# Kernel optimization log

Hardware: AMD Instinct MI355X
Metric: run time of the kernel (lower is better)

## Reference

```python
import jax, jax.numpy as jnp
import numpy as np

N, E = 10000, 80000
D, D_EDGE, L = 32, 16, 3
D2 = D * D


def layer_norm(x, g, b, eps=1e-5):
    m = jnp.mean(x, axis=-1, keepdims=True)
    v = jnp.var(x, axis=-1, keepdims=True)
    return (x - m) / jnp.sqrt(v + eps) * g + b


def setup_inputs() -> dict:
    key = jax.random.key(0)
    ks = jax.random.split(key, 16)
    s_e = 1.0 / np.sqrt(D_EDGE)
    s_d = 1.0 / np.sqrt(D)
    s_f = 1.0 / np.sqrt(L * D)
    return {
        "x": jax.random.normal(ks[0], (N, D), dtype=jnp.float32),
        "edge_index": jax.random.randint(ks[1], (2, E), 0, N),
        "edge_attr": jax.random.normal(ks[2], (E, D_EDGE), dtype=jnp.float32),
        # shared edge MLP: Linear(d_edge_in -> d^2) + LayerNorm(d^2) + ReLU
        "emlp_w": jax.random.uniform(ks[3], (D2, D_EDGE), jnp.float32, -s_e, s_e),
        "emlp_b": jnp.zeros((D2,), jnp.float32),
        "emlp_ln_g": jnp.ones((D2,), jnp.float32),
        "emlp_ln_b": jnp.zeros((D2,), jnp.float32),
        # per-layer params (stacked over L layers)
        "root_w": jax.random.uniform(ks[4], (L, D, D), jnp.float32, -s_d, s_d),  # NNConv root lin (no bias)
        "conv_b": jnp.zeros((L, D), jnp.float32),                                # NNConv bias
        "res_w": jax.random.uniform(ks[5], (L, D, D), jnp.float32, -s_d, s_d),
        "res_b": jnp.zeros((L, D), jnp.float32),
        "ln_g": jnp.ones((L, D), jnp.float32),
        "ln_b": jnp.zeros((L, D), jnp.float32),
        # fusion: Linear(L*d -> d) + LayerNorm(d) + ReLU
        "fuse_w": jax.random.uniform(ks[6], (D, L * D), jnp.float32, -s_f, s_f),
        "fuse_b": jnp.zeros((D,), jnp.float32),
        "fuse_ln_g": jnp.ones((D,), jnp.float32),
        "fuse_ln_b": jnp.zeros((D,), jnp.float32),
    }


def reference(x, edge_index, edge_attr, emlp_w, emlp_b, emlp_ln_g, emlp_ln_b,
              root_w, conv_b, res_w, res_b, ln_g, ln_b,
              fuse_w, fuse_b, fuse_ln_g, fuse_ln_b):
    n_nodes = x.shape[0]
    src, tgt = edge_index[0], edge_index[1]
    # Shared edge MLP applied to the same edge_attr in every layer -> identical
    # per-edge weight matrices; compute once. [E, d_in, d_out]
    h = layer_norm(edge_attr @ emlp_w.T + emlp_b, emlp_ln_g, emlp_ln_b)
    We = jax.nn.relu(h).reshape(-1, D, D)
    x_src_gatherer = src
    outputs = []
    for l in range(L):
        x_res = x @ res_w[l].T + res_b[l]
        # NNConv message: x_j @ W_e, scatter-add to target nodes
        msg = jnp.einsum('ed,edf->ef', x[x_src_gatherer], We)  # [E, d]
        agg = jax.ops.segment_sum(msg, tgt, num_segments=n_nodes)
        h = agg + x @ root_w[l].T + conv_b[l]
        # dropout is identity in eval mode
        x = layer_norm(h + x_res, ln_g[l], ln_b[l])
        outputs.append(x)
    fused = jnp.concatenate(outputs, axis=-1) @ fuse_w.T + fuse_b
    fused = jax.nn.relu(layer_norm(fused, fuse_ln_g, fuse_ln_b))
    return fused
```

## Files before the change

kernel.cpp:

```cpp
#include <hip/hip_runtime.h>

#define NN 10000
#define EE 80000
#define DD 32
#define DEDGE 16
#define LL 3
#define D2V 1024
#define NTILE 2500

typedef __attribute__((ext_vector_type(8))) short short8v;
typedef __attribute__((ext_vector_type(16))) float f32x16;

__device__ __forceinline__ unsigned short bf16rne(float x) {
    unsigned u = __float_as_uint(x);
    return (unsigned short)((u + 0x7FFF + ((u >> 16) & 1)) >> 16);
}
__device__ __forceinline__ float bf16tof(unsigned short h) {
    return __uint_as_float(((unsigned)h) << 16);
}
__device__ __forceinline__ uint4 pack8(const unsigned short* u) {
    uint4 r;
    r.x = (unsigned)u[0] | ((unsigned)u[1] << 16);
    r.y = (unsigned)u[2] | ((unsigned)u[3] << 16);
    r.z = (unsigned)u[4] | ((unsigned)u[5] << 16);
    r.w = (unsigned)u[6] | ((unsigned)u[7] << 16);
    return r;
}

__global__ __launch_bounds__(1024) void setup_kernel(
    const int* __restrict__ ei,
    const float* __restrict__ emw, const float* __restrict__ emb,
    const float* __restrict__ elg, const float* __restrict__ elb,
    int* __restrict__ cur, int* __restrict__ off, float* __restrict__ st,
    uint4* __restrict__ afh, uint4* __restrict__ afl, uint4* __restrict__ a2f)
{
    __shared__ int smi[NN + 1024];
    const int bid = blockIdx.x;
    const int t = threadIdx.x;

    if (bid == 0) {
        int* cnt = smi;
        int* part = smi + NN;
        for (int i = t; i < NN; i += 1024) cnt[i] = 0;
        __syncthreads();
        for (int e = t; e < EE; e += 1024) atomicAdd(&cnt[ei[EE + e]], 1);
        __syncthreads();
        const int base = t * 10;
        int loc[10];
        int run = 0;
#pragma unroll
        for (int i = 0; i < 10; ++i) {
            const int idx = base + i;
            const int v = (idx < NN) ? cnt[idx] : 0;
            loc[i] = run;
            run += v;
        }
        part[t] = run;
        __syncthreads();
        for (int o = 1; o < 1024; o <<= 1) {
            const int v = (t >= o) ? part[t - o] : 0;
            __syncthreads();
            part[t] += v;
            __syncthreads();
        }
        const int excl = part[t] - run;
#pragma unroll
        for (int i = 0; i < 10; ++i) {
            const int idx = base + i;
            if (idx < NN) {
                off[idx] = excl + loc[i];
                cur[idx] = excl + loc[i];
            }
        }
        if (t == 1023) off[NN] = part[1023];
    } else if (bid == 1) {
        float* ws = (float*)smi;
        float* bs = ((float*)smi) + 2048;
        float accM = 0.f, s = 0.f, q = 0.f, sb = 0.f, sb2 = 0.f;
        for (int c = 0; c < 8; ++c) {
            const int r0 = c * 128;
            for (int i = t; i < 2048; i += 1024) ws[i] = emw[r0 * DEDGE + i];
            if (t < 128) bs[t] = emb[r0 + t];
            __syncthreads();
            if (t < 256) {
                const int k = t >> 4, j = t & 15;
                for (int r = 0; r < 128; ++r)
                    accM = fmaf(ws[r * 16 + k], ws[r * 16 + j], accM);
            } else if (t < 272) {
                const int kk = t - 256;
                for (int r = 0; r < 128; ++r) {
                    s += ws[r * 16 + kk];
                    q = fmaf(bs[r], ws[r * 16 + kk], q);
                }
            } else if (t == 288) {
                for (int r = 0; r < 128; ++r) {
                    sb += bs[r];
                    sb2 = fmaf(bs[r], bs[r], sb2);
                }
            }
            __syncthreads();
        }
        if (t < 256) {
            st[t] = accM * (1.f / D2V);
        } else if (t < 272) {
            st[t] = s * (1.f / D2V);
            st[t + 16] = q * (1.f / D2V);
        } else if (t == 288) {
            st[288] = sb * (1.f / D2V);
            st[289] = sb2 * (1.f / D2V);
        }
    } else {
        const int tid2 = (bid - 2) * 1024 + t;
        const int d = tid2 >> 6, l = tid2 & 63;
        const int row = l & 31, kh = l >> 5;
        const int r = d * 32 + row;
        const float g = elg[r];
        unsigned short uh[8], ul[8];
#pragma unroll
        for (int i = 0; i < 8; ++i) {
            const float v = g * emw[r * DEDGE + kh * 8 + i];
            const unsigned short h = bf16rne(v);
            uh[i] = h;
            ul[i] = bf16rne(v - bf16tof(h));
        }
        afh[d * 64 + l] = pack8(uh);
        afl[d * 64 + l] = pack8(ul);
        if (kh == 0) {
            const float bg = g * emb[r];
            const float lbv = elb[r];
            const unsigned short bgh = bf16rne(bg);
            const unsigned short bgl = bf16rne(bg - bf16tof(bgh));
            const unsigned short gh = bf16rne(g);
            const unsigned short gl = bf16rne(g - bf16tof(gh));
            const unsigned short lbh = bf16rne(lbv);
            const unsigned short lbl = bf16rne(lbv - bf16tof(lbh));
            unsigned short sarr[8] = {bgh, bgl, bgh, gh, gl, gh, lbh, lbl};
            a2f[d * 64 + l] = pack8(sarr);
        } else {
            a2f[d * 64 + l] = make_uint4(0, 0, 0, 0);
        }
    }
}

__global__ __launch_bounds__(256) void stats_edge_perm2(const float* __restrict__ eattr,
                                                        const float* __restrict__ st,
                                                        const int* __restrict__ ei,
                                                        int* __restrict__ cur,
                                                        uint4* __restrict__ bfh,
                                                        uint4* __restrict__ bfl,
                                                        uint4* __restrict__ b2f,
                                                        int* __restrict__ sperm) {
    const int e = blockIdx.x * 256 + threadIdx.x;
    if (e >= EE) return;
    const int tgt = ei[EE + e];
    const int p = atomicAdd(&cur[tgt], 1);
    sperm[p] = ei[e];
    float ea[16];
    {
        const float4* ep = (const float4*)(eattr + e * DEDGE);
#pragma unroll
        for (int c = 0; c < 4; ++c) {
            const float4 t4 = ep[c];
            ea[4 * c] = t4.x; ea[4 * c + 1] = t4.y; ea[4 * c + 2] = t4.z; ea[4 * c + 3] = t4.w;
        }
    }
    float m = st[288];
#pragma unroll
    for (int k = 0; k < 16; ++k) m = fmaf(st[256 + k], ea[k], m);
    float ex2 = st[289];
#pragma unroll
    for (int k = 0; k < 16; ++k) {
        float tv = 2.f * st[272 + k];
#pragma unroll
        for (int j = 0; j < 16; ++j) tv = fmaf(st[k * 16 + j], ea[j], tv);
        ex2 = fmaf(tv, ea[k], ex2);
    }
    const float var = fmaxf(ex2 - m * m, 0.f);
    const float inv = rsqrtf(var + 1e-5f);
    const float nmi = -m * inv;
    const int tt = p >> 5, col = p & 31;
#pragma unroll
    for (int h = 0; h < 2; ++h) {
        unsigned short uh[8], ul[8];
#pragma unroll
        for (int i = 0; i < 8; ++i) {
            const float v = inv * ea[8 * h + i];
            const unsigned short a = bf16rne(v);
            uh[i] = a;
            ul[i] = bf16rne(v - bf16tof(a));
        }
        bfh[tt * 64 + h * 32 + col] = pack8(uh);
        bfl[tt * 64 + h * 32 + col] = pack8(ul);
    }
    const unsigned short ivh = bf16rne(inv);
    const unsigned short ivl = bf16rne(inv - bf16tof(ivh));
    const unsigned short nmh = bf16rne(nmi);
    const unsigned short nml = bf16rne(nmi - bf16tof(nmh));
    const unsigned short one = 0x3F80;
    unsigned short s[8] = {ivh, ivh, ivl, nmh, nmh, nml, one, one};
    b2f[tt * 64 + col] = pack8(s);
    b2f[tt * 64 + 32 + col] = make_uint4(0, 0, 0, 0);
}

__global__ __launch_bounds__(256) void edge_mfma_kernel(
    const float* __restrict__ x, const int* __restrict__ sperm,
    const uint4* __restrict__ afh, const uint4* __restrict__ afl, const uint4* __restrict__ a2f,
    const uint4* __restrict__ bfh, const uint4* __restrict__ bfl, const uint4* __restrict__ b2f,
    float* __restrict__ msgout) {
    const int lane = threadIdx.x & 63;
    const int w = (blockIdx.x * 256 + threadIdx.x) >> 6;
    const int col = lane & 31, hi = lane >> 5;
    const int p = w * 32 + col;
    const int si = sperm[p];
    float xr[32];
    {
        const float4* xp = (const float4*)(x + si * DD);
#pragma unroll
        for (int c = 0; c < 8; ++c) {
            const float4 t4 = xp[c];
            xr[4 * c] = t4.x; xr[4 * c + 1] = t4.y; xr[4 * c + 2] = t4.z; xr[4 * c + 3] = t4.w;
        }
    }
    const short8v bh = ((const short8v*)bfh)[w * 64 + lane];
    const short8v bl = ((const short8v*)bfl)[w * 64 + lane];
    const short8v b2 = ((const short8v*)b2f)[w * 64 + lane];
    float mg[16];
#pragma unroll
    for (int i = 0; i < 16; ++i) mg[i] = 0.f;
#pragma unroll
    for (int d = 0; d < 32; ++d) {
        const short8v ah = ((const short8v*)afh)[d * 64 + lane];
        const short8v al = ((const short8v*)afl)[d * 64 + lane];
        const short8v a2 = ((const short8v*)a2f)[d * 64 + lane];
        f32x16 C;
#pragma unroll
        for (int r = 0; r < 16; ++r) C[r] = 0.f;
        C = __builtin_amdgcn_mfma_f32_32x32x16_bf16(ah, bh, C, 0, 0, 0);
        C = __builtin_amdgcn_mfma_f32_32x32x16_bf16(ah, bl, C, 0, 0, 0);
        C = __builtin_amdgcn_mfma_f32_32x32x16_bf16(al, bh, C, 0, 0, 0);
        C = __builtin_amdgcn_mfma_f32_32x32x16_bf16(a2, b2, C, 0, 0, 0);
        const float xd = xr[d];
#pragma unroll
        for (int r = 0; r < 16; ++r) mg[r] = fmaf(xd, fmaxf(C[r], 0.f), mg[r]);
    }
    float* op = msgout + p * DD + hi * 4;
#pragma unroll
    for (int q = 0; q < 4; ++q)
        *(float4*)(op + q * 8) = make_float4(mg[4 * q], mg[4 * q + 1], mg[4 * q + 2], mg[4 * q + 3]);
}

__global__ __launch_bounds__(256) void node_wave_kernel(
    const float* __restrict__ x, const float* __restrict__ msg,
    const int* __restrict__ off,
    const float* __restrict__ root_w, const float* __restrict__ conv_b,
    const float* __restrict__ res_w, const float* __restrict__ res_b,
    const float* __restrict__ lng, const float* __restrict__ lnb,
    float* __restrict__ out) {
    const int lane = threadIdx.x & 63;
    const int w = (blockIdx.x * 256 + threadIdx.x) >> 6;
    const int hi = lane >> 5, f = lane & 31;
    const int n = w * 2 + hi;
    float wrow[32];
    {
        const float4* rp = (const float4*)(root_w + f * DD);
        const float4* sp = (const float4*)(res_w + f * DD);
#pragma unroll
        for (int c = 0; c < 8; ++c) {
            const float4 a = rp[c];
            const float4 b = sp[c];
            wrow[4 * c] = a.x + b.x; wrow[4 * c + 1] = a.y + b.y;
            wrow[4 * c + 2] = a.z + b.z; wrow[4 * c + 3] = a.w + b.w;
        }
    }
    float acc = conv_b[f] + res_b[f];
    const int k0 = off[n], k1 = off[n + 1];
    for (int k = k0; k < k1; ++k) acc += msg[k * DD + f];
    const float xl = x[n * DD + f];
#pragma unroll
    for (int d = 0; d < DD; ++d) acc = fmaf(__shfl(xl, hi * 32 + d), wrow[d], acc);
    float s1 = acc, s2 = acc * acc;
#pragma unroll
    for (int o = 16; o >= 1; o >>= 1) {
        s1 += __shfl_xor(s1, o);
        s2 += __shfl_xor(s2, o);
    }
    const float m = s1 * (1.f / 32.f);
    const float v = s2 * (1.f / 32.f) - m * m;
    const float inv = rsqrtf(v + 1e-5f);
    out[n * DD + f] = fmaf((acc - m) * inv, lng[f], lnb[f]);
}

__global__ __launch_bounds__(256) void node_fuse_kernel(
    const float* __restrict__ x, const float* __restrict__ msg,
    const int* __restrict__ off,
    const float* __restrict__ root_w, const float* __restrict__ conv_b,
    const float* __restrict__ res_w, const float* __restrict__ res_b,
    const float* __restrict__ lng, const float* __restrict__ lnb,
    const float* __restrict__ o0, const float* __restrict__ o1,
    const float* __restrict__ fw, const float* __restrict__ fb,
    const float* __restrict__ fg, const float* __restrict__ fbb,
    float* __restrict__ out) {
    const int lane = threadIdx.x & 63;
    const int w = (blockIdx.x * 256 + threadIdx.x) >> 6;
    const int hi = lane >> 5, f = lane & 31;
    const int n = w * 2 + hi;
    float o2v;
    {
        float wrow[32];
        {
            const float4* rp = (const float4*)(root_w + f * DD);
            const float4* sp = (const float4*)(res_w + f * DD);
#pragma unroll
            for (int c = 0; c < 8; ++c) {
                const float4 a = rp[c];
                const float4 b = sp[c];
                wrow[4 * c] = a.x + b.x; wrow[4 * c + 1] = a.y + b.y;
                wrow[4 * c + 2] = a.z + b.z; wrow[4 * c + 3] = a.w + b.w;
            }
        }
        float acc = conv_b[f] + res_b[f];
        const int k0 = off[n], k1 = off[n + 1];
        for (int k = k0; k < k1; ++k) acc += msg[k * DD + f];
        const float xl = x[n * DD + f];
#pragma unroll
        for (int d = 0; d < DD; ++d) acc = fmaf(__shfl(xl, hi * 32 + d), wrow[d], acc);
        float s1 = acc, s2 = acc * acc;
#pragma unroll
        for (int o = 16; o >= 1; o >>= 1) {
            s1 += __shfl_xor(s1, o);
            s2 += __shfl_xor(s2, o);
        }
        const float m = s1 * (1.f / 32.f);
        const float v = s2 * (1.f / 32.f) - m * m;
        const float inv = rsqrtf(v + 1e-5f);
        o2v = fmaf((acc - m) * inv, lng[f], lnb[f]);
    }
    float fr[96];
    {
        const float4* fp = (const float4*)(fw + f * 96);
#pragma unroll
        for (int c = 0; c < 24; ++c) {
            const float4 t4 = fp[c];
            fr[4 * c] = t4.x; fr[4 * c + 1] = t4.y; fr[4 * c + 2] = t4.z; fr[4 * c + 3] = t4.w;
        }
    }
    float acc = fb[f];
    const float c0 = o0[n * DD + f], c1 = o1[n * DD + f];
#pragma unroll
    for (int d = 0; d < DD; ++d) acc = fmaf(__shfl(c0, hi * 32 + d), fr[d], acc);
#pragma unroll
    for (int d = 0; d < DD; ++d) acc = fmaf(__shfl(c1, hi * 32 + d), fr[32 + d], acc);
#pragma unroll
    for (int d = 0; d < DD; ++d) acc = fmaf(__shfl(o2v, hi * 32 + d), fr[64 + d], acc);
    float s1 = acc, s2 = acc * acc;
#pragma unroll
    for (int o = 16; o >= 1; o >>= 1) {
        s1 += __shfl_xor(s1, o);
        s2 += __shfl_xor(s2, o);
    }
    const float m = s1 * (1.f / 32.f);
    const float v = s2 * (1.f / 32.f) - m * m;
    const float inv = rsqrtf(v + 1e-5f);
    out[n * DD + f] = fmaxf(fmaf((acc - m) * inv, fg[f], fbb[f]), 0.f);
}

extern "C" void kernel_launch(void* const* d_in, const int* in_sizes, int n_in,
                              void* d_out, int out_size, void* d_ws, size_t ws_size,
                              hipStream_t stream) {
    const float* x   = (const float*)d_in[0];
    const int*   ei  = (const int*)d_in[1];
    const float* ea  = (const float*)d_in[2];
    const float* emw = (const float*)d_in[3];
    const float* emb = (const float*)d_in[4];
    const float* elg = (const float*)d_in[5];
    const float* elb = (const float*)d_in[6];
    const float* rootw = (const float*)d_in[7];
    const float* convb = (const float*)d_in[8];
    const float* resw  = (const float*)d_in[9];
    const float* resb  = (const float*)d_in[10];
    const float* lng   = (const float*)d_in[11];
    const float* lnb   = (const float*)d_in[12];
    const float* fw    = (const float*)d_in[13];
    const float* fb    = (const float*)d_in[14];
    const float* flg   = (const float*)d_in[15];
    const float* flb   = (const float*)d_in[16];
    float* doutp = (float*)d_out;

    const size_t U4N = 2048 * 3 + (size_t)NTILE * 64 * 3;
    const size_t FR0 = U4N * 4;
    const size_t FTOT = FR0 + (size_t)EE * DD + 2 * (size_t)NN * DD + 320;
    const size_t ITOT = 2 * (NN + 1) + 2 * (size_t)EE;
    const size_t PRIMARY_NEED = FTOT * 4 + ITOT * 4 + 256;

    if (ws_size < PRIMARY_NEED) return;

    uint4* u4 = (uint4*)d_ws;
    uint4* afh = u4;
    uint4* afl = afh + 2048;
    uint4* a2f = afl + 2048;
    uint4* bfh = a2f + 2048;
    uint4* bfl = bfh + (size_t)NTILE * 64;
    uint4* b2f = bfl + (size_t)NTILE * 64;
    float* wsf = (float*)d_ws;
    float* msg  = wsf + FR0;
    float* out0 = msg + (size_t)EE * DD;
    float* out1 = out0 + NN * DD;
    float* st   = out1 + NN * DD;
    int* cur   = (int*)(st + 320);
    int* off   = cur + (NN + 1);
    int* spare = off + (NN + 1);
    int* sperm = spare + EE;
    (void)spare;

    setup_kernel<<<4, 1024, 0, stream>>>(ei, emw, emb, elg, elb, cur, off, st,
                                         afh, afl, a2f);
    stats_edge_perm2<<<313, 256, 0, stream>>>(ea, st, ei, cur, bfh, bfl, b2f, sperm);

    edge_mfma_kernel<<<625, 256, 0, stream>>>(x, sperm, afh, afl, a2f, bfh, bfl, b2f, msg);
    node_wave_kernel<<<1250, 256, 0, stream>>>(x, msg, off,
        rootw, convb, resw, resb, lng, lnb, out0);
    edge_mfma_kernel<<<625, 256, 0, stream>>>(out0, sperm, afh, afl, a2f, bfh, bfl, b2f, msg);
    node_wave_kernel<<<1250, 256, 0, stream>>>(out0, msg, off,
        rootw + D2V, convb + DD, resw + D2V, resb + DD, lng + DD, lnb + DD, out1);
    edge_mfma_kernel<<<625, 256, 0, stream>>>(out1, sperm, afh, afl, a2f, bfh, bfl, b2f, msg);
    node_fuse_kernel<<<1250, 256, 0, stream>>>(out1, msg, off,
        rootw + 2 * D2V, convb + 2 * DD, resw + 2 * D2V, resb + 2 * DD,
        lng + 2 * DD, lnb + 2 * DD,
        out0, out1, fw, fb, flg, flb, doutp);
}
```

Measured before the change: 174.8 us.

## Stage edge-MLP weight fragments in LDS and parallelize degree counting

The edge message kernel now runs 512-thread blocks that first copy the bf16 hi/lo weight fragments and a compacted bias/scale fragment into shared memory. The MFMA loop then reads them from LDS instead of re-fetching them from global memory in every wave. Target-degree counting moves from one shared-memory block to global atomics spread over 313 blocks, preceded by a memset and followed by a separate single-block scan kernel. The cost is about 80KB of LDS per block, which limits occupancy, plus two extra launches in the setup phase.

```diff
diff --git a/kernel.cpp b/kernel.cpp
--- a/kernel.cpp
+++ b/kernel.cpp
@@ -27,72 +27,34 @@
     return r;
 }
 
-__global__ __launch_bounds__(1024) void setup_kernel(
+__global__ __launch_bounds__(256) void setup322_kernel(
     const int* __restrict__ ei,
-    const float* __restrict__ emw, const float* __restrict__ emb,
-    const float* __restrict__ elg, const float* __restrict__ elb,
-    int* __restrict__ cur, int* __restrict__ off, float* __restrict__ st,
-    uint4* __restrict__ afh, uint4* __restrict__ afl, uint4* __restrict__ a2f)
-{
-    __shared__ int smi[NN + 1024];
+    const float* __restrict__ w, const float* __restrict__ wb,
+    const float* __restrict__ lg, const float* __restrict__ lb,
+    int* __restrict__ cnt, float* __restrict__ st,
+    uint4* __restrict__ afh, uint4* __restrict__ afl, uint4* __restrict__ a2c) {
+    __shared__ float ws[2048];
+    __shared__ float bs[128];
     const int bid = blockIdx.x;
     const int t = threadIdx.x;
-
-    if (bid == 0) {
-        int* cnt = smi;
-        int* part = smi + NN;
-        for (int i = t; i < NN; i += 1024) cnt[i] = 0;
-        __syncthreads();
-        for (int e = t; e < EE; e += 1024) atomicAdd(&cnt[ei[EE + e]], 1);
-        __syncthreads();
-        const int base = t * 10;
-        int loc[10];
-        int run = 0;
-#pragma unroll
-        for (int i = 0; i < 10; ++i) {
-            const int idx = base + i;
-            const int v = (idx < NN) ? cnt[idx] : 0;
-            loc[i] = run;
-            run += v;
-        }
-        part[t] = run;
-        __syncthreads();
-        for (int o = 1; o < 1024; o <<= 1) {
-            const int v = (t >= o) ? part[t - o] : 0;
+    if (bid < 313) {
+        const int e = bid * 256 + t;
+        if (e < EE) atomicAdd(&cnt[ei[EE + e]], 1);
+    } else if (bid == 313) {
+        float accM = 0.f, s = 0.f, q = 0.f, sb = 0.f, sb2 = 0.f;
+        const int k = t >> 4, j = t & 15;
+        for (int c = 0; c < 8; ++c) {
+            for (int i = t; i < 2048; i += 256) ws[i] = w[c * 2048 + i];
+            if (t < 128) bs[t] = wb[c * 128 + t];
             __syncthreads();
-            part[t] += v;
-            __syncthreads();
-        }
-        const int excl = part[t] - run;
-#pragma unroll
-        for (int i = 0; i < 10; ++i) {
-            const int idx = base + i;
-            if (idx < NN) {
-                off[idx] = excl + loc[i];
-                cur[idx] = excl + loc[i];
-            }
-        }
-        if (t == 1023) off[NN] = part[1023];
-    } else if (bid == 1) {
-        float* ws = (float*)smi;
-        float* bs = ((float*)smi) + 2048;
-        float accM = 0.f, s = 0.f, q = 0.f, sb = 0.f, sb2 = 0.f;
-        for (int c = 0; c < 8; ++c) {
-            const int r0 = c * 128;
-            for (int i = t; i < 2048; i += 1024) ws[i] = emw[r0 * DEDGE + i];
-            if (t < 128) bs[t] = emb[r0 + t];
-            __syncthreads();
-            if (t < 256) {
-                const int k = t >> 4, j = t & 15;
-                for (int r = 0; r < 128; ++r)
-                    accM = fmaf(ws[r * 16 + k], ws[r * 16 + j], accM);
-            } else if (t < 272) {
-                const int kk = t - 256;
+            for (int r = 0; r < 128; ++r)
+                accM = fmaf(ws[r * 16 + k], ws[r * 16 + j], accM);
+            if (t < DEDGE) {
                 for (int r = 0; r < 128; ++r) {
-                    s += ws[r * 16 + kk];
-                    q = fmaf(bs[r], ws[r * 16 + kk], q);
+                    s += ws[r * 16 + t];
+                    q = fmaf(bs[r], ws[r * 16 + t], q);
                 }
-            } else if (t == 288) {
+            } else if (t == 16) {
                 for (int r = 0; r < 128; ++r) {
                     sb += bs[r];
                     sb2 = fmaf(bs[r], bs[r], sb2);
@@ -100,25 +62,24 @@
             }
             __syncthreads();
         }
-        if (t < 256) {
-            st[t] = accM * (1.f / D2V);
-        } else if (t < 272) {
-            st[t] = s * (1.f / D2V);
-            st[t + 16] = q * (1.f / D2V);
-        } else if (t == 288) {
+        st[t] = accM * (1.f / D2V);
+        if (t < DEDGE) {
+            st[256 + t] = s * (1.f / D2V);
+            st[272 + t] = q * (1.f / D2V);
+        } else if (t == 16) {
             st[288] = sb * (1.f / D2V);
             st[289] = sb2 * (1.f / D2V);
         }
     } else {
-        const int tid2 = (bid - 2) * 1024 + t;
+        const int tid2 = (bid - 314) * 256 + t;
         const int d = tid2 >> 6, l = tid2 & 63;
         const int row = l & 31, kh = l >> 5;
         const int r = d * 32 + row;
-        const float g = elg[r];
+        const float g = lg[r];
         unsigned short uh[8], ul[8];
 #pragma unroll
         for (int i = 0; i < 8; ++i) {
-            const float v = g * emw[r * DEDGE + kh * 8 + i];
+            const float v = g * w[r * DEDGE + kh * 8 + i];
             const unsigned short h = bf16rne(v);
             uh[i] = h;
             ul[i] = bf16rne(v - bf16tof(h));
@@ -126,8 +87,8 @@
         afh[d * 64 + l] = pack8(uh);
         afl[d * 64 + l] = pack8(ul);
         if (kh == 0) {
-            const float bg = g * emb[r];
-            const float lbv = elb[r];
+            const float bg = g * wb[r];
+            const float lbv = lb[r];
             const unsigned short bgh = bf16rne(bg);
             const unsigned short bgl = bf16rne(bg - bf16tof(bgh));
             const unsigned short gh = bf16rne(g);
@@ -135,11 +96,42 @@
             const unsigned short lbh = bf16rne(lbv);
             const unsigned short lbl = bf16rne(lbv - bf16tof(lbh));
             unsigned short sarr[8] = {bgh, bgl, bgh, gh, gl, gh, lbh, lbl};
-            a2f[d * 64 + l] = pack8(sarr);
-        } else {
-            a2f[d * 64 + l] = make_uint4(0, 0, 0, 0);
-        }
-    }
+            a2c[d * 32 + row] = pack8(sarr);
+        }
+    }
+}
+
+__global__ __launch_bounds__(1024) void scan_kernel(int* __restrict__ cur, int* __restrict__ off) {
+    __shared__ int s[1024];
+    const int t = threadIdx.x;
+    const int base = t * 10;
+    int loc[10];
+    int run = 0;
+#pragma unroll
+    for (int i = 0; i < 10; ++i) {
+        const int idx = base + i;
+        const int v = (idx < NN) ? cur[idx] : 0;
+        loc[i] = run;
+        run += v;
+    }
+    s[t] = run;
+    __syncthreads();
+    for (int o = 1; o < 1024; o <<= 1) {
+        const int v = (t >= o) ? s[t - o] : 0;
+        __syncthreads();
+        s[t] += v;
+        __syncthreads();
+    }
+    const int excl = s[t] - run;
+#pragma unroll
+    for (int i = 0; i < 10; ++i) {
+        const int idx = base + i;
+        if (idx < NN) {
+            off[idx] = excl + loc[i];
+            cur[idx] = excl + loc[i];
+        }
+    }
+    if (t == 1023) off[NN] = s[1023];
 }
 
 __global__ __launch_bounds__(256) void stats_edge_perm2(const float* __restrict__ eattr,
@@ -202,13 +194,25 @@
     b2f[tt * 64 + 32 + col] = make_uint4(0, 0, 0, 0);
 }
 
-__global__ __launch_bounds__(256) void edge_mfma_kernel(
+__global__ __launch_bounds__(512) void edge_mfma_lds(
     const float* __restrict__ x, const int* __restrict__ sperm,
-    const uint4* __restrict__ afh, const uint4* __restrict__ afl, const uint4* __restrict__ a2f,
+    const uint4* __restrict__ afh, const uint4* __restrict__ afl, const uint4* __restrict__ a2c,
     const uint4* __restrict__ bfh, const uint4* __restrict__ bfl, const uint4* __restrict__ b2f,
     float* __restrict__ msgout) {
-    const int lane = threadIdx.x & 63;
-    const int w = (blockIdx.x * 256 + threadIdx.x) >> 6;
+    __shared__ uint4 lafh[2048];
+    __shared__ uint4 lafl[2048];
+    __shared__ uint4 la2c[1024];
+    const int t = threadIdx.x;
+    for (int i = t; i < 2048; i += 512) {
+        lafh[i] = afh[i];
+        lafl[i] = afl[i];
+    }
+    for (int i = t; i < 1024; i += 512) la2c[i] = a2c[i];
+    __syncthreads();
+
+    const int lane = t & 63;
+    const int w = blockIdx.x * 8 + (t >> 6);
+    if (w >= NTILE) return;
     const int col = lane & 31, hi = lane >> 5;
     const int p = w * 32 + col;
     const int si = sperm[p];
@@ -229,9 +233,9 @@
     for (int i = 0; i < 16; ++i) mg[i] = 0.f;
 #pragma unroll
     for (int d = 0; d < 32; ++d) {
-        const short8v ah = ((const short8v*)afh)[d * 64 + lane];
-        const short8v al = ((const short8v*)afl)[d * 64 + lane];
-        const short8v a2 = ((const short8v*)a2f)[d * 64 + lane];
+        const short8v ah = ((const short8v*)lafh)[d * 64 + lane];
+        const short8v al = ((const short8v*)lafl)[d * 64 + lane];
+        const short8v a2 = ((const short8v*)la2c)[d * 32 + col];
         f32x16 C;
 #pragma unroll
         for (int r = 0; r < 16; ++r) C[r] = 0.f;
@@ -397,8 +401,8 @@
     uint4* u4 = (uint4*)d_ws;
     uint4* afh = u4;
     uint4* afl = afh + 2048;
-    uint4* a2f = afl + 2048;
-    uint4* bfh = a2f + 2048;
+    uint4* a2c = afl + 2048;
+    uint4* bfh = a2c + 2048;
     uint4* bfl = bfh + (size_t)NTILE * 64;
     uint4* b2f = bfl + (size_t)NTILE * 64;
     float* wsf = (float*)d_ws;
@@ -412,17 +416,18 @@
     int* sperm = spare + EE;
     (void)spare;
 
-    setup_kernel<<<4, 1024, 0, stream>>>(ei, emw, emb, elg, elb, cur, off, st,
-                                         afh, afl, a2f);
+    hipMemsetAsync(cur, 0, (NN + 1) * sizeof(int), stream);
+    setup322_kernel<<<322, 256, 0, stream>>>(ei, emw, emb, elg, elb, cur, st, afh, afl, a2c);
+    scan_kernel<<<1, 1024, 0, stream>>>(cur, off);
     stats_edge_perm2<<<313, 256, 0, stream>>>(ea, st, ei, cur, bfh, bfl, b2f, sperm);
 
-    edge_mfma_kernel<<<625, 256, 0, stream>>>(x, sperm, afh, afl, a2f, bfh, bfl, b2f, msg);
+    edge_mfma_lds<<<313, 512, 0, stream>>>(x, sperm, afh, afl, a2c, bfh, bfl, b2f, msg);
     node_wave_kernel<<<1250, 256, 0, stream>>>(x, msg, off,
         rootw, convb, resw, resb, lng, lnb, out0);
-    edge_mfma_kernel<<<625, 256, 0, stream>>>(out0, sperm, afh, afl, a2f, bfh, bfl, b2f, msg);
+    edge_mfma_lds<<<313, 512, 0, stream>>>(out0, sperm, afh, afl, a2c, bfh, bfl, b2f, msg);
     node_wave_kernel<<<1250, 256, 0, stream>>>(out0, msg, off,
         rootw + D2V, convb + DD, resw + D2V, resb + DD, lng + DD, lnb + DD, out1);
-    edge_mfma_kernel<<<625, 256, 0, stream>>>(out1, sperm, afh, afl, a2f, bfh, bfl, b2f, msg);
+    edge_mfma_lds<<<313, 512, 0, stream>>>(out1, sperm, afh, afl, a2c, bfh, bfl, b2f, msg);
     node_fuse_kernel<<<1250, 256, 0, stream>>>(out1, msg, off,
         rootw + 2 * D2V, convb + 2 * DD, resw + 2 * D2V, resb + 2 * DD,
         lng + 2 * DD, lnb + 2 * DD,
```

Measured after the change: 199.3 us. 14.0% more time.
